# Optimization experiments

Hardware: AMD Instinct MI355X
Metric: run time of the kernel (lower is better)

The kernel has to match this reference:

```python
import jax, jax.numpy as jnp
import numpy as np

N_TOKENS = 8192
EMBED = 1024
HIDDEN = 4 * EMBED
NUM_EXPERTS = 8


def setup_inputs() -> dict:
    key = jax.random.key(0)
    ks = jax.random.split(key, 10)
    s = 0.02
    return {
        "x": jax.random.normal(ks[0], (N_TOKENS, EMBED), dtype=jnp.float32),
        # Router params
        "Wr1": jax.random.normal(ks[1], (EMBED, EMBED), dtype=jnp.float32) * s,
        "br1": jnp.zeros((EMBED,), dtype=jnp.float32),
        "Wr2": jax.random.normal(ks[2], (EMBED, NUM_EXPERTS), dtype=jnp.float32) * s,
        "br2": jnp.zeros((NUM_EXPERTS,), dtype=jnp.float32),
        # Expert FFN params, stacked over experts
        "W1": jax.random.normal(ks[3], (NUM_EXPERTS, EMBED, HIDDEN), dtype=jnp.float32) * s,
        "b1": jnp.zeros((NUM_EXPERTS, HIDDEN), dtype=jnp.float32),
        "W2": jax.random.normal(ks[4], (NUM_EXPERTS, HIDDEN, EMBED), dtype=jnp.float32) * s,
        "b2": jnp.zeros((NUM_EXPERTS, EMBED), dtype=jnp.float32),
    }


def reference(x, Wr1, br1, Wr2, br2, W1, b1, W2, b2):
    # Router: Linear -> ReLU -> Linear -> softmax over experts -> top-1
    h = jax.nn.relu(x @ Wr1 + br1)                      # [N, E]
    probs = jax.nn.softmax(h @ Wr2 + br2, axis=1)       # [N, num_experts]
    chosen = jnp.argmax(probs, axis=1)                  # [N]

    num_experts = W1.shape[0]
    out = jnp.zeros_like(x)
    # Fixed small loop over experts (structurally distinct weights).
    for e in range(num_experts):
        ffn_e = jax.nn.relu(x @ W1[e] + b1[e]) @ W2[e] + b2[e]  # [N, E]
        out = jnp.where((chosen == e)[:, None], ffn_e, out)
    # Note: original returns raw expert output (no probability weighting).
    return out
```

## Files before the change

kernel.cpp:

```cpp
#include <hip/hip_runtime.h>
#include <stdint.h>

#define N_TOK 8192
#define EMB 1024
#define HID 4096
#define NEXP 8

typedef _Float16 f16x8 __attribute__((ext_vector_type(8)));
typedef _Float16 f16x4 __attribute__((ext_vector_type(4)));
typedef short    s16x8 __attribute__((ext_vector_type(8)));
typedef unsigned short u16x8 __attribute__((ext_vector_type(8)));
typedef float    f32x4 __attribute__((ext_vector_type(4)));

typedef __attribute__((address_space(1))) const void gvoid_t;
typedef __attribute__((address_space(3))) void lvoid_t;

__device__ __forceinline__ void async16(const void* g, void* l) {
  __builtin_amdgcn_global_load_lds((gvoid_t*)g, (lvoid_t*)l, 16, 0, 0);
}

__device__ __forceinline__ unsigned short f2bf(float f) {
  unsigned u = __builtin_bit_cast(unsigned, f);
  u += 0x7fffu + ((u >> 16) & 1u);
  return (unsigned short)(u >> 16);
}

__global__ __launch_bounds__(256) void k_cast_x(const float* __restrict__ x,
    unsigned short* __restrict__ xb, _Float16* __restrict__ xhi, _Float16* __restrict__ xlo) {
  int i = (blockIdx.x * 256 + threadIdx.x) << 2;
  float4 v = *(const float4*)(x + i);
  ushort4 b;
  b.x = f2bf(v.x); b.y = f2bf(v.y); b.z = f2bf(v.z); b.w = f2bf(v.w);
  *(ushort4*)(xb + i) = b;
  float vv[4] = {v.x, v.y, v.z, v.w};
  f16x4 hi, lo;
#pragma unroll
  for (int j = 0; j < 4; j++) {
    _Float16 h = (_Float16)vv[j];
    hi[j] = h;
    lo[j] = (_Float16)(vv[j] - (float)h);
  }
  *(f16x4*)(xhi + i) = hi;
  *(f16x4*)(xlo + i) = lo;
}

__global__ __launch_bounds__(256) void k_trans_wr1(const float* __restrict__ src,
    _Float16* __restrict__ dhi, _Float16* __restrict__ dlo) {
  int nblk = blockIdx.x >> 4, kc = blockIdx.x & 15;
  int n = (nblk << 8) + threadIdx.x;
  int k0 = kc << 6;
  for (int k = k0; k < k0 + 64; k += 8) {
    f16x8 hi, lo;
#pragma unroll
    for (int j = 0; j < 8; j++) {
      float w = src[(size_t)(k + j) * EMB + n] * 256.0f;
      _Float16 h = (_Float16)w;
      hi[j] = h;
      lo[j] = (_Float16)(w - (float)h);
    }
    *(f16x8*)(dhi + (size_t)n * EMB + k) = hi;
    *(f16x8*)(dlo + (size_t)n * EMB + k) = lo;
  }
}

__global__ __launch_bounds__(256) void k_transcast_v2(const float* __restrict__ src,
    unsigned short* __restrict__ dst, int K, int Nn, int ktiles, int ntiles) {
  __shared__ __align__(16) unsigned short lds[256 * 72];
  int b = blockIdx.x;
  int e = b / (ktiles * ntiles);
  int r = b % (ktiles * ntiles);
  int kt = r / ntiles, nt = r % ntiles;
  int k0 = kt << 6, n0 = nt << 8;
  const float* s = src + (size_t)e * K * Nn;
  unsigned short* d = dst + (size_t)e * K * Nn;
  int tid = threadIdx.x;
  const float* scol = s + n0 + tid;
#pragma unroll 4
  for (int k = 0; k < 64; k += 2) {
    float a  = scol[(size_t)(k0 + k) * Nn];
    float bv = scol[(size_t)(k0 + k + 1) * Nn];
    unsigned p = (unsigned)f2bf(a) | ((unsigned)f2bf(bv) << 16);
    *(unsigned*)(lds + tid * 72 + k) = p;
  }
  __syncthreads();
  int c = tid & 7, nl = tid >> 3;
#pragma unroll
  for (int p2 = 0; p2 < 8; p2++) {
    int n = (p2 << 5) + nl;
    u16x8 v = *(const u16x8*)(lds + n * 72 + (c << 3));
    *(u16x8*)(d + (size_t)(n0 + n) * K + k0 + (c << 3)) = v;
  }
}

__global__ __launch_bounds__(256) void k_router_gemm(
    const _Float16* __restrict__ Ah, const _Float16* __restrict__ Al,
    const _Float16* __restrict__ Bh, const _Float16* __restrict__ Bl,
    const float* __restrict__ br1, float* __restrict__ hOut) {
  __shared__ __align__(16) _Float16 sAh[4096], sAl[4096], sBh[4096], sBl[4096];
  const int tid = threadIdx.x, lane = tid & 63, wave = tid >> 6;
  const int m0 = (blockIdx.x >> 3) << 7;
  const int n0 = (blockIdx.x & 7) << 7;
  const int srow = (wave << 5) + (lane >> 2);
  const int scol = (lane & 3) << 3;
  const size_t aBase = (size_t)(m0 + srow) * EMB + scol;
  const size_t bBase = (size_t)(n0 + srow) * EMB + scol;
  _Float16* lAh = sAh + (wave << 10);
  _Float16* lAl = sAl + (wave << 10);
  _Float16* lBh = sBh + (wave << 10);
  _Float16* lBl = sBl + (wave << 10);
  const int q = lane >> 4, c = lane & 15;
  const int msub = (wave & 1) << 6, nsub = (wave >> 1) << 6;
  f32x4 acc[4][4];
#pragma unroll
  for (int i = 0; i < 4; i++)
#pragma unroll
    for (int j = 0; j < 4; j++) acc[i][j] = (f32x4){0.f, 0.f, 0.f, 0.f};

  for (int kk = 0; kk < EMB; kk += 32) {
    async16(Ah + aBase + kk, lAh);
    async16(Ah + aBase + 16 * EMB + kk, lAh + 512);
    async16(Al + aBase + kk, lAl);
    async16(Al + aBase + 16 * EMB + kk, lAl + 512);
    async16(Bh + bBase + kk, lBh);
    async16(Bh + bBase + 16 * EMB + kk, lBh + 512);
    async16(Bl + bBase + kk, lBl);
    async16(Bl + bBase + 16 * EMB + kk, lBl + 512);
    __syncthreads();
    f16x8 fah[4], fal[4], fbh[4], fbl[4];
#pragma unroll
    for (int i = 0; i < 4; i++) {
      int ar = msub + (i << 4) + c;
      int br = nsub + (i << 4) + c;
      fah[i] = *(const f16x8*)(sAh + (ar << 5) + (q << 3));
      fal[i] = *(const f16x8*)(sAl + (ar << 5) + (q << 3));
      fbh[i] = *(const f16x8*)(sBh + (br << 5) + (q << 3));
      fbl[i] = *(const f16x8*)(sBl + (br << 5) + (q << 3));
    }
#pragma unroll
    for (int mi = 0; mi < 4; mi++)
#pragma unroll
      for (int ni = 0; ni < 4; ni++) {
        acc[mi][ni] = __builtin_amdgcn_mfma_f32_16x16x32_f16(fah[mi], fbh[ni], acc[mi][ni], 0, 0, 0);
        acc[mi][ni] = __builtin_amdgcn_mfma_f32_16x16x32_f16(fah[mi], fbl[ni], acc[mi][ni], 0, 0, 0);
        acc[mi][ni] = __builtin_amdgcn_mfma_f32_16x16x32_f16(fal[mi], fbh[ni], acc[mi][ni], 0, 0, 0);
      }
    __syncthreads();
  }
#pragma unroll
  for (int mi = 0; mi < 4; mi++)
#pragma unroll
    for (int ni = 0; ni < 4; ni++) {
      int gn = n0 + nsub + (ni << 4) + c;
      float bias = 256.0f * br1[gn];
#pragma unroll
      for (int i2 = 0; i2 < 4; i2++) {
        int gm = m0 + msub + (mi << 4) + (q << 2) + i2;
        float v = acc[mi][ni][i2] + bias;
        hOut[(size_t)gm * EMB + gn] = v > 0.f ? v : 0.f;
      }
    }
}

__global__ __launch_bounds__(256) void k_logits(const float* __restrict__ h,
    const float* __restrict__ Wr2, const float* __restrict__ br2, int* __restrict__ chosen) {
  __shared__ __align__(16) float sW[EMB * NEXP];
  int tid = threadIdx.x;
  for (int i = tid; i < EMB * NEXP; i += 256) sW[i] = Wr2[i];
  __syncthreads();
  int lane = tid & 63, wave = tid >> 6;
  int t = blockIdx.x * 4 + wave;
  const float* hr = h + (size_t)t * EMB;
  float acc[8] = {0.f, 0.f, 0.f, 0.f, 0.f, 0.f, 0.f, 0.f};
#pragma unroll
  for (int i = 0; i < 16; i++) {
    int k = (i << 6) + lane;
    float v = hr[k];
    float4 w0 = *(const float4*)(sW + (k << 3));
    float4 w1 = *(const float4*)(sW + (k << 3) + 4);
    acc[0] += v * w0.x; acc[1] += v * w0.y; acc[2] += v * w0.z; acc[3] += v * w0.w;
    acc[4] += v * w1.x; acc[5] += v * w1.y; acc[6] += v * w1.z; acc[7] += v * w1.w;
  }
#pragma unroll
  for (int off = 32; off > 0; off >>= 1)
#pragma unroll
    for (int e = 0; e < 8; e++) acc[e] += __shfl_down(acc[e], off);
  if (lane == 0) {
    float best = acc[0] + 256.0f * br2[0];
    int bi = 0;
#pragma unroll
    for (int e = 1; e < 8; e++) {
      float l = acc[e] + 256.0f * br2[e];
      if (l > best) { best = l; bi = e; }
    }
    chosen[t] = bi;
  }
}

__global__ void k_zero(int* meta) { meta[threadIdx.x] = 0; }

__global__ __launch_bounds__(256) void k_hist(const int* __restrict__ chosen, int* meta) {
  int i = blockIdx.x * 256 + threadIdx.x;
  atomicAdd(&meta[chosen[i]], 1);
}

__global__ __launch_bounds__(128) void k_sched(int* meta) {
  __shared__ int cnt[8];
  int tid = threadIdx.x;
  if (tid < 8) cnt[tid] = meta[tid];
  __syncthreads();
  int off[9]; off[0] = 0;
#pragma unroll
  for (int e = 0; e < 8; e++) off[e + 1] = off[e] + cnt[e];
  int ts[9]; ts[0] = 0;
#pragma unroll
  for (int e = 0; e < 8; e++) ts[e + 1] = ts[e] + ((cnt[e] + 127) >> 7);
  int T = ts[8];
  if (tid < 8) meta[16 + tid] = off[tid];
  if (tid == 0) { meta[24] = off[8]; meta[25] = T; }
  if (tid < T) {
    int e = 0;
    while (ts[e + 1] <= tid) e++;
    int m = off[e] + ((tid - ts[e]) << 7);
    int end = off[e + 1];
    meta[32 + tid] = e;
    meta[112 + tid] = m;
    meta[192 + tid] = (m + 128 < end) ? m + 128 : end;
  }
}

__global__ __launch_bounds__(256) void k_scatter(const int* __restrict__ chosen,
                                                 int* meta, int* __restrict__ perm) {
  int i = blockIdx.x * 256 + threadIdx.x;
  int e = chosen[i];
  int pos = meta[16 + e] + atomicAdd(&meta[8 + e], 1);
  perm[pos] = i;
}

__global__ __launch_bounds__(256) void k_ffn1(
    const unsigned short* __restrict__ xb, const unsigned short* __restrict__ w1t,
    const float* __restrict__ b1, const int* __restrict__ perm,
    const int* __restrict__ meta, unsigned short* __restrict__ hidden) {
  const int mt = blockIdx.x >> 5;
  if (mt >= meta[25]) return;
  const int nt = blockIdx.x & 31;
  const int e = meta[32 + mt];
  const int row0 = meta[112 + mt];
  const int rend = meta[192 + mt];
  const int n0 = nt << 7;
  __shared__ __align__(16) unsigned short sA[4096], sB[4096];
  const int tid = threadIdx.x, lane = tid & 63, wave = tid >> 6;
  const int srow = (wave << 5) + (lane >> 2);
  const int scol = (lane & 3) << 3;
  int ra0 = row0 + srow, ra1 = row0 + srow + 16;
  if (ra0 > rend - 1) ra0 = rend - 1;
  if (ra1 > rend - 1) ra1 = rend - 1;
  const int t0 = perm[ra0], t1 = perm[ra1];
  const unsigned short* a0 = xb + (size_t)t0 * EMB + scol;
  const unsigned short* a1 = xb + (size_t)t1 * EMB + scol;
  const unsigned short* bsrc = w1t + (size_t)e * EMB * HID + (size_t)(n0 + srow) * EMB + scol;
  unsigned short* lA = sA + (wave << 10);
  unsigned short* lB = sB + (wave << 10);
  const int q = lane >> 4, c = lane & 15;
  const int msub = (wave & 1) << 6, nsub = (wave >> 1) << 6;
  f32x4 acc[4][4];
#pragma unroll
  for (int i = 0; i < 4; i++)
#pragma unroll
    for (int j = 0; j < 4; j++) acc[i][j] = (f32x4){0.f, 0.f, 0.f, 0.f};

  for (int kk = 0; kk < EMB; kk += 32) {
    async16(a0 + kk, lA);
    async16(a1 + kk, lA + 512);
    async16(bsrc + kk, lB);
    async16(bsrc + 16 * EMB + kk, lB + 512);
    __syncthreads();
    s16x8 fa[4], fb[4];
#pragma unroll
    for (int i = 0; i < 4; i++) {
      fa[i] = *(const s16x8*)(sA + ((msub + (i << 4) + c) << 5) + (q << 3));
      fb[i] = *(const s16x8*)(sB + ((nsub + (i << 4) + c) << 5) + (q << 3));
    }
#pragma unroll
    for (int mi = 0; mi < 4; mi++)
#pragma unroll
      for (int ni = 0; ni < 4; ni++)
        acc[mi][ni] = __builtin_amdgcn_mfma_f32_16x16x32_bf16(fa[mi], fb[ni], acc[mi][ni], 0, 0, 0);
    __syncthreads();
  }
#pragma unroll
  for (int mi = 0; mi < 4; mi++)
#pragma unroll
    for (int ni = 0; ni < 4; ni++) {
      int gn = n0 + nsub + (ni << 4) + c;
      float bias = b1[e * HID + gn];
#pragma unroll
      for (int i2 = 0; i2 < 4; i2++) {
        int rs = row0 + msub + (mi << 4) + (q << 2) + i2;
        if (rs < rend) {
          float v = acc[mi][ni][i2] + bias;
          v = v > 0.f ? v : 0.f;
          hidden[(size_t)rs * HID + gn] = f2bf(v);
        }
      }
    }
}

__global__ __launch_bounds__(256) void k_ffn2(
    const unsigned short* __restrict__ hidden, const unsigned short* __restrict__ w2t,
    const float* __restrict__ b2, const int* __restrict__ perm,
    const int* __restrict__ meta, float* __restrict__ out) {
  const int mt = blockIdx.x >> 3;
  if (mt >= meta[25]) return;
  const int nt = blockIdx.x & 7;
  const int e = meta[32 + mt];
  const int row0 = meta[112 + mt];
  const int rend = meta[192 + mt];
  const int n0 = nt << 7;
  __shared__ __align__(16) unsigned short sA[4096], sB[4096];
  const int tid = threadIdx.x, lane = tid & 63, wave = tid >> 6;
  const int srow = (wave << 5) + (lane >> 2);
  const int scol = (lane & 3) << 3;
  int ra0 = row0 + srow, ra1 = row0 + srow + 16;
  if (ra0 > N_TOK - 1) ra0 = N_TOK - 1;
  if (ra1 > N_TOK - 1) ra1 = N_TOK - 1;
  const unsigned short* a0 = hidden + (size_t)ra0 * HID + scol;
  const unsigned short* a1 = hidden + (size_t)ra1 * HID + scol;
  const unsigned short* bsrc = w2t + (size_t)e * HID * EMB + (size_t)(n0 + srow) * HID + scol;
  unsigned short* lA = sA + (wave << 10);
  unsigned short* lB = sB + (wave << 10);
  const int q = lane >> 4, c = lane & 15;
  const int msub = (wave & 1) << 6, nsub = (wave >> 1) << 6;
  f32x4 acc[4][4];
#pragma unroll
  for (int i = 0; i < 4; i++)
#pragma unroll
    for (int j = 0; j < 4; j++) acc[i][j] = (f32x4){0.f, 0.f, 0.f, 0.f};

  for (int kk = 0; kk < HID; kk += 32) {
    async16(a0 + kk, lA);
    async16(a1 + kk, lA + 512);
    async16(bsrc + kk, lB);
    async16(bsrc + 16 * HID + kk, lB + 512);
    __syncthreads();
    s16x8 fa[4], fb[4];
#pragma unroll
    for (int i = 0; i < 4; i++) {
      fa[i] = *(const s16x8*)(sA + ((msub + (i << 4) + c) << 5) + (q << 3));
      fb[i] = *(const s16x8*)(sB + ((nsub + (i << 4) + c) << 5) + (q << 3));
    }
#pragma unroll
    for (int mi = 0; mi < 4; mi++)
#pragma unroll
      for (int ni = 0; ni < 4; ni++)
        acc[mi][ni] = __builtin_amdgcn_mfma_f32_16x16x32_bf16(fa[mi], fb[ni], acc[mi][ni], 0, 0, 0);
    __syncthreads();
  }
#pragma unroll
  for (int mi = 0; mi < 4; mi++)
#pragma unroll
    for (int ni = 0; ni < 4; ni++) {
      int gn = n0 + nsub + (ni << 4) + c;
      float bias = b2[e * EMB + gn];
#pragma unroll
      for (int i2 = 0; i2 < 4; i2++) {
        int rs = row0 + msub + (mi << 4) + (q << 2) + i2;
        if (rs < rend) {
          int orig = perm[rs];
          out[(size_t)orig * EMB + gn] = acc[mi][ni][i2] + bias;
        }
      }
    }
}

extern "C" void kernel_launch(void* const* d_in, const int* in_sizes, int n_in,
                              void* d_out, int out_size, void* d_ws, size_t ws_size,
                              hipStream_t stream) {
  const float* x   = (const float*)d_in[0];
  const float* Wr1 = (const float*)d_in[1];
  const float* br1 = (const float*)d_in[2];
  const float* Wr2 = (const float*)d_in[3];
  const float* br2 = (const float*)d_in[4];
  const float* W1  = (const float*)d_in[5];
  const float* b1  = (const float*)d_in[6];
  const float* W2  = (const float*)d_in[7];
  const float* b2  = (const float*)d_in[8];
  float* out = (float*)d_out;
  char* ws = (char*)d_ws;

  unsigned short* w1t    = (unsigned short*)(ws + 0);
  unsigned short* w2t    = (unsigned short*)(ws + 67108864);
  unsigned short* xb     = (unsigned short*)(ws + 134217728);
  _Float16*       xhi    = (_Float16*)(ws + 150994944);
  _Float16*       xlo    = (_Float16*)(ws + 167772160);
  _Float16*       whi    = (_Float16*)(ws + 184549376);
  _Float16*       wlo    = (_Float16*)(ws + 186646528);
  float*          hbuf   = (float*)(ws + 188743680);
  unsigned short* hidden = (unsigned short*)(ws + 222298112);
  int*            chosen = (int*)(ws + 289406976);
  int*            perm   = (int*)(ws + 289439744);
  int*            meta   = (int*)(ws + 289472512);

  k_cast_x<<<dim3(8192), dim3(256), 0, stream>>>(x, xb, xhi, xlo);
  k_trans_wr1<<<dim3(64), dim3(256), 0, stream>>>(Wr1, whi, wlo);
  k_transcast_v2<<<dim3(2048), dim3(256), 0, stream>>>(W1, w1t, 1024, 4096, 16, 16);
  k_transcast_v2<<<dim3(2048), dim3(256), 0, stream>>>(W2, w2t, 4096, 1024, 64, 4);
  k_router_gemm<<<dim3(512), dim3(256), 0, stream>>>(xhi, xlo, whi, wlo, br1, hbuf);
  k_logits<<<dim3(2048), dim3(256), 0, stream>>>(hbuf, Wr2, br2, chosen);
  k_zero<<<dim3(1), dim3(256), 0, stream>>>(meta);
  k_hist<<<dim3(32), dim3(256), 0, stream>>>(chosen, meta);
  k_sched<<<dim3(1), dim3(128), 0, stream>>>(meta);
  k_scatter<<<dim3(32), dim3(256), 0, stream>>>(chosen, meta, perm);
  k_ffn1<<<dim3(2304), dim3(256), 0, stream>>>(xb, w1t, b1, perm, meta, hidden);
  k_ffn2<<<dim3(576), dim3(256), 0, stream>>>(hidden, w2t, b2, perm, meta, out);
}
```

Baseline: 773.3 us.

## Software-pipeline GEMM loads with multi-buffered LDS and remap block order

Router, FFN1 and FFN2 GEMMs now prefetch the next K-slice into a second (or, for FFN2, a ring of four) LDS buffer via async global-to-LDS loads. Explicit vmcnt waits and raw s_barrier replace __syncthreads so memory latency overlaps MFMA work. Block indices are also remapped so consecutive workgroups spread across N tiles, likely to improve cache sharing across XCDs. The cost is double or quadruple LDS use, which may lower occupancy. FFN2 drops the trailing barrier and relies on the four-buffer ring to avoid overwrite races.

```diff
diff --git a/kernel.cpp b/kernel.cpp
--- a/kernel.cpp
+++ b/kernel.cpp
@@ -96,18 +96,16 @@
     const _Float16* __restrict__ Ah, const _Float16* __restrict__ Al,
     const _Float16* __restrict__ Bh, const _Float16* __restrict__ Bl,
     const float* __restrict__ br1, float* __restrict__ hOut) {
-  __shared__ __align__(16) _Float16 sAh[4096], sAl[4096], sBh[4096], sBl[4096];
+  __shared__ __align__(16) _Float16 sAh[2][4096], sAl[2][4096], sBh[2][4096], sBl[2][4096];
+  const int wg = (blockIdx.x & 7) * 64 + (blockIdx.x >> 3);
   const int tid = threadIdx.x, lane = tid & 63, wave = tid >> 6;
-  const int m0 = (blockIdx.x >> 3) << 7;
-  const int n0 = (blockIdx.x & 7) << 7;
+  const int m0 = (wg >> 3) << 7;
+  const int n0 = (wg & 7) << 7;
   const int srow = (wave << 5) + (lane >> 2);
   const int scol = (lane & 3) << 3;
   const size_t aBase = (size_t)(m0 + srow) * EMB + scol;
   const size_t bBase = (size_t)(n0 + srow) * EMB + scol;
-  _Float16* lAh = sAh + (wave << 10);
-  _Float16* lAl = sAl + (wave << 10);
-  _Float16* lBh = sBh + (wave << 10);
-  _Float16* lBl = sBl + (wave << 10);
+  const int lofs = wave << 10;
   const int q = lane >> 4, c = lane & 15;
   const int msub = (wave & 1) << 6, nsub = (wave >> 1) << 6;
   f32x4 acc[4][4];
@@ -116,25 +114,37 @@
 #pragma unroll
     for (int j = 0; j < 4; j++) acc[i][j] = (f32x4){0.f, 0.f, 0.f, 0.f};
 
-  for (int kk = 0; kk < EMB; kk += 32) {
-    async16(Ah + aBase + kk, lAh);
-    async16(Ah + aBase + 16 * EMB + kk, lAh + 512);
-    async16(Al + aBase + kk, lAl);
-    async16(Al + aBase + 16 * EMB + kk, lAl + 512);
-    async16(Bh + bBase + kk, lBh);
-    async16(Bh + bBase + 16 * EMB + kk, lBh + 512);
-    async16(Bl + bBase + kk, lBl);
-    async16(Bl + bBase + 16 * EMB + kk, lBl + 512);
-    __syncthreads();
+#define RSTAGE(kk, b) do { \
+    async16(Ah + aBase + (kk), sAh[b] + lofs); \
+    async16(Ah + aBase + 16 * EMB + (kk), sAh[b] + lofs + 512); \
+    async16(Al + aBase + (kk), sAl[b] + lofs); \
+    async16(Al + aBase + 16 * EMB + (kk), sAl[b] + lofs + 512); \
+    async16(Bh + bBase + (kk), sBh[b] + lofs); \
+    async16(Bh + bBase + 16 * EMB + (kk), sBh[b] + lofs + 512); \
+    async16(Bl + bBase + (kk), sBl[b] + lofs); \
+    async16(Bl + bBase + 16 * EMB + (kk), sBl[b] + lofs + 512); } while (0)
+
+  RSTAGE(0, 0);
+  const int nk = EMB / 32;
+  for (int t = 0; t < nk; ++t) {
+    const int b = t & 1;
+    if (t + 1 < nk) {
+      RSTAGE((t + 1) << 5, b ^ 1);
+      asm volatile("s_waitcnt vmcnt(8)" ::: "memory");
+    } else {
+      asm volatile("s_waitcnt vmcnt(0)" ::: "memory");
+    }
+    __builtin_amdgcn_s_barrier();
+    asm volatile("" ::: "memory");
     f16x8 fah[4], fal[4], fbh[4], fbl[4];
 #pragma unroll
     for (int i = 0; i < 4; i++) {
       int ar = msub + (i << 4) + c;
       int br = nsub + (i << 4) + c;
-      fah[i] = *(const f16x8*)(sAh + (ar << 5) + (q << 3));
-      fal[i] = *(const f16x8*)(sAl + (ar << 5) + (q << 3));
-      fbh[i] = *(const f16x8*)(sBh + (br << 5) + (q << 3));
-      fbl[i] = *(const f16x8*)(sBl + (br << 5) + (q << 3));
+      fah[i] = *(const f16x8*)(sAh[b] + (ar << 5) + (q << 3));
+      fal[i] = *(const f16x8*)(sAl[b] + (ar << 5) + (q << 3));
+      fbh[i] = *(const f16x8*)(sBh[b] + (br << 5) + (q << 3));
+      fbl[i] = *(const f16x8*)(sBl[b] + (br << 5) + (q << 3));
     }
 #pragma unroll
     for (int mi = 0; mi < 4; mi++)
@@ -144,8 +154,10 @@
         acc[mi][ni] = __builtin_amdgcn_mfma_f32_16x16x32_f16(fah[mi], fbl[ni], acc[mi][ni], 0, 0, 0);
         acc[mi][ni] = __builtin_amdgcn_mfma_f32_16x16x32_f16(fal[mi], fbh[ni], acc[mi][ni], 0, 0, 0);
       }
-    __syncthreads();
-  }
+    asm volatile("" ::: "memory");
+    __builtin_amdgcn_s_barrier();
+  }
+#undef RSTAGE
 #pragma unroll
   for (int mi = 0; mi < 4; mi++)
 #pragma unroll
@@ -240,14 +252,15 @@
     const unsigned short* __restrict__ xb, const unsigned short* __restrict__ w1t,
     const float* __restrict__ b1, const int* __restrict__ perm,
     const int* __restrict__ meta, unsigned short* __restrict__ hidden) {
-  const int mt = blockIdx.x >> 5;
+  const int wg = (blockIdx.x & 7) * 288 + (blockIdx.x >> 3);
+  const int mt = wg >> 5;
   if (mt >= meta[25]) return;
-  const int nt = blockIdx.x & 31;
+  const int nt = wg & 31;
   const int e = meta[32 + mt];
   const int row0 = meta[112 + mt];
   const int rend = meta[192 + mt];
   const int n0 = nt << 7;
-  __shared__ __align__(16) unsigned short sA[4096], sB[4096];
+  __shared__ __align__(16) unsigned short sA[2][4096], sB[2][4096];
   const int tid = threadIdx.x, lane = tid & 63, wave = tid >> 6;
   const int srow = (wave << 5) + (lane >> 2);
   const int scol = (lane & 3) << 3;
@@ -258,8 +271,7 @@
   const unsigned short* a0 = xb + (size_t)t0 * EMB + scol;
   const unsigned short* a1 = xb + (size_t)t1 * EMB + scol;
   const unsigned short* bsrc = w1t + (size_t)e * EMB * HID + (size_t)(n0 + srow) * EMB + scol;
-  unsigned short* lA = sA + (wave << 10);
-  unsigned short* lB = sB + (wave << 10);
+  const int lofs = wave << 10;
   const int q = lane >> 4, c = lane & 15;
   const int msub = (wave & 1) << 6, nsub = (wave >> 1) << 6;
   f32x4 acc[4][4];
@@ -268,25 +280,39 @@
 #pragma unroll
     for (int j = 0; j < 4; j++) acc[i][j] = (f32x4){0.f, 0.f, 0.f, 0.f};
 
-  for (int kk = 0; kk < EMB; kk += 32) {
-    async16(a0 + kk, lA);
-    async16(a1 + kk, lA + 512);
-    async16(bsrc + kk, lB);
-    async16(bsrc + 16 * EMB + kk, lB + 512);
-    __syncthreads();
+#define F1STAGE(kk, b) do { \
+    async16(a0 + (kk), sA[b] + lofs); \
+    async16(a1 + (kk), sA[b] + lofs + 512); \
+    async16(bsrc + (kk), sB[b] + lofs); \
+    async16(bsrc + 16 * EMB + (kk), sB[b] + lofs + 512); } while (0)
+
+  F1STAGE(0, 0);
+  const int nk = EMB / 32;
+  for (int t = 0; t < nk; ++t) {
+    const int b = t & 1;
+    if (t + 1 < nk) {
+      F1STAGE((t + 1) << 5, b ^ 1);
+      asm volatile("s_waitcnt vmcnt(4)" ::: "memory");
+    } else {
+      asm volatile("s_waitcnt vmcnt(0)" ::: "memory");
+    }
+    __builtin_amdgcn_s_barrier();
+    asm volatile("" ::: "memory");
     s16x8 fa[4], fb[4];
 #pragma unroll
     for (int i = 0; i < 4; i++) {
-      fa[i] = *(const s16x8*)(sA + ((msub + (i << 4) + c) << 5) + (q << 3));
-      fb[i] = *(const s16x8*)(sB + ((nsub + (i << 4) + c) << 5) + (q << 3));
+      fa[i] = *(const s16x8*)(sA[b] + ((msub + (i << 4) + c) << 5) + (q << 3));
+      fb[i] = *(const s16x8*)(sB[b] + ((nsub + (i << 4) + c) << 5) + (q << 3));
     }
 #pragma unroll
     for (int mi = 0; mi < 4; mi++)
 #pragma unroll
       for (int ni = 0; ni < 4; ni++)
         acc[mi][ni] = __builtin_amdgcn_mfma_f32_16x16x32_bf16(fa[mi], fb[ni], acc[mi][ni], 0, 0, 0);
-    __syncthreads();
-  }
+    asm volatile("" ::: "memory");
+    __builtin_amdgcn_s_barrier();
+  }
+#undef F1STAGE
 #pragma unroll
   for (int mi = 0; mi < 4; mi++)
 #pragma unroll
@@ -309,14 +335,15 @@
     const unsigned short* __restrict__ hidden, const unsigned short* __restrict__ w2t,
     const float* __restrict__ b2, const int* __restrict__ perm,
     const int* __restrict__ meta, float* __restrict__ out) {
-  const int mt = blockIdx.x >> 3;
+  const int wg = (blockIdx.x & 7) * 72 + (blockIdx.x >> 3);
+  const int mt = wg >> 3;
   if (mt >= meta[25]) return;
-  const int nt = blockIdx.x & 7;
+  const int nt = wg & 7;
   const int e = meta[32 + mt];
   const int row0 = meta[112 + mt];
   const int rend = meta[192 + mt];
   const int n0 = nt << 7;
-  __shared__ __align__(16) unsigned short sA[4096], sB[4096];
+  __shared__ __align__(16) unsigned short sA[4][4096], sB[4][4096];
   const int tid = threadIdx.x, lane = tid & 63, wave = tid >> 6;
   const int srow = (wave << 5) + (lane >> 2);
   const int scol = (lane & 3) << 3;
@@ -326,8 +353,7 @@
   const unsigned short* a0 = hidden + (size_t)ra0 * HID + scol;
   const unsigned short* a1 = hidden + (size_t)ra1 * HID + scol;
   const unsigned short* bsrc = w2t + (size_t)e * HID * EMB + (size_t)(n0 + srow) * HID + scol;
-  unsigned short* lA = sA + (wave << 10);
-  unsigned short* lB = sB + (wave << 10);
+  const int lofs = wave << 10;
   const int q = lane >> 4, c = lane & 15;
   const int msub = (wave & 1) << 6, nsub = (wave >> 1) << 6;
   f32x4 acc[4][4];
@@ -336,25 +362,41 @@
 #pragma unroll
     for (int j = 0; j < 4; j++) acc[i][j] = (f32x4){0.f, 0.f, 0.f, 0.f};
 
-  for (int kk = 0; kk < HID; kk += 32) {
-    async16(a0 + kk, lA);
-    async16(a1 + kk, lA + 512);
-    async16(bsrc + kk, lB);
-    async16(bsrc + 16 * HID + kk, lB + 512);
-    __syncthreads();
+#define F2STAGE(kk, b) do { \
+    async16(a0 + (kk), sA[b] + lofs); \
+    async16(a1 + (kk), sA[b] + lofs + 512); \
+    async16(bsrc + (kk), sB[b] + lofs); \
+    async16(bsrc + 16 * HID + (kk), sB[b] + lofs + 512); } while (0)
+
+  F2STAGE(0, 0);
+  F2STAGE(32, 1);
+  const int nk = HID / 32;
+#pragma unroll 1
+  for (int t = 0; t < nk; ++t) {
+    const int b = t & 3;
+    if (t + 2 < nk) {
+      F2STAGE((t + 2) << 5, (t + 2) & 3);
+      asm volatile("s_waitcnt vmcnt(8)" ::: "memory");
+    } else if (t + 1 < nk) {
+      asm volatile("s_waitcnt vmcnt(4)" ::: "memory");
+    } else {
+      asm volatile("s_waitcnt vmcnt(0)" ::: "memory");
+    }
+    __builtin_amdgcn_s_barrier();
+    asm volatile("" ::: "memory");
     s16x8 fa[4], fb[4];
 #pragma unroll
     for (int i = 0; i < 4; i++) {
-      fa[i] = *(const s16x8*)(sA + ((msub + (i << 4) + c) << 5) + (q << 3));
-      fb[i] = *(const s16x8*)(sB + ((nsub + (i << 4) + c) << 5) + (q << 3));
+      fa[i] = *(const s16x8*)(sA[b] + ((msub + (i << 4) + c) << 5) + (q << 3));
+      fb[i] = *(const s16x8*)(sB[b] + ((nsub + (i << 4) + c) << 5) + (q << 3));
     }
 #pragma unroll
     for (int mi = 0; mi < 4; mi++)
 #pragma unroll
       for (int ni = 0; ni < 4; ni++)
         acc[mi][ni] = __builtin_amdgcn_mfma_f32_16x16x32_bf16(fa[mi], fb[ni], acc[mi][ni], 0, 0, 0);
-    __syncthreads();
-  }
+  }
+#undef F2STAGE
 #pragma unroll
   for (int mi = 0; mi < 4; mi++)
 #pragma unroll
```

After: 823.8 us. 6.5% more time.

## Double-buffer FFN GEMM LDS tiles, XOR-swizzle LDS, remap blocks for L2 locality

Applied to the files above, without the earlier changes.

The FFN1 and FFN2 expert GEMMs now double-buffer their LDS tiles, prefetching the next K-slice with async global-to-LDS loads while MFMAs run on the current one, with one wait and barrier per iteration. Column offsets are XOR-swizzled so fragment reads avoid LDS bank conflicts. FFN2 also doubles its K-step to 64 to halve the number of barriers. Block indices in the router and FFN kernels are remapped so that consecutive blocks spread across eight groups, aiming for better L2 reuse. The cost is twice the LDS per block, which may lower occupancy.

```diff
diff --git a/kernel.cpp b/kernel.cpp
--- a/kernel.cpp
+++ b/kernel.cpp
@@ -97,9 +97,10 @@
     const _Float16* __restrict__ Bh, const _Float16* __restrict__ Bl,
     const float* __restrict__ br1, float* __restrict__ hOut) {
   __shared__ __align__(16) _Float16 sAh[4096], sAl[4096], sBh[4096], sBl[4096];
+  const int wg = (blockIdx.x & 7) * 64 + (blockIdx.x >> 3);
   const int tid = threadIdx.x, lane = tid & 63, wave = tid >> 6;
-  const int m0 = (blockIdx.x >> 3) << 7;
-  const int n0 = (blockIdx.x & 7) << 7;
+  const int m0 = (wg >> 3) << 7;
+  const int n0 = (wg & 7) << 7;
   const int srow = (wave << 5) + (lane >> 2);
   const int scol = (lane & 3) << 3;
   const size_t aBase = (size_t)(m0 + srow) * EMB + scol;
@@ -240,17 +241,18 @@
     const unsigned short* __restrict__ xb, const unsigned short* __restrict__ w1t,
     const float* __restrict__ b1, const int* __restrict__ perm,
     const int* __restrict__ meta, unsigned short* __restrict__ hidden) {
-  const int mt = blockIdx.x >> 5;
+  const int wg = (blockIdx.x & 7) * 288 + (blockIdx.x >> 3);
+  const int mt = wg >> 5;
   if (mt >= meta[25]) return;
-  const int nt = blockIdx.x & 31;
+  const int nt = wg & 31;
   const int e = meta[32 + mt];
   const int row0 = meta[112 + mt];
   const int rend = meta[192 + mt];
   const int n0 = nt << 7;
-  __shared__ __align__(16) unsigned short sA[4096], sB[4096];
+  __shared__ __align__(16) unsigned short sA[2][4096], sB[2][4096];
   const int tid = threadIdx.x, lane = tid & 63, wave = tid >> 6;
   const int srow = (wave << 5) + (lane >> 2);
-  const int scol = (lane & 3) << 3;
+  const int scol = (((lane & 3) ^ ((lane >> 2) & 3)) << 3);
   int ra0 = row0 + srow, ra1 = row0 + srow + 16;
   if (ra0 > rend - 1) ra0 = rend - 1;
   if (ra1 > rend - 1) ra1 = rend - 1;
@@ -258,35 +260,45 @@
   const unsigned short* a0 = xb + (size_t)t0 * EMB + scol;
   const unsigned short* a1 = xb + (size_t)t1 * EMB + scol;
   const unsigned short* bsrc = w1t + (size_t)e * EMB * HID + (size_t)(n0 + srow) * EMB + scol;
-  unsigned short* lA = sA + (wave << 10);
-  unsigned short* lB = sB + (wave << 10);
+  const int lofs = wave << 10;
   const int q = lane >> 4, c = lane & 15;
   const int msub = (wave & 1) << 6, nsub = (wave >> 1) << 6;
+  const int cs = ((q ^ (c & 3)) << 3);
   f32x4 acc[4][4];
 #pragma unroll
   for (int i = 0; i < 4; i++)
 #pragma unroll
     for (int j = 0; j < 4; j++) acc[i][j] = (f32x4){0.f, 0.f, 0.f, 0.f};
 
-  for (int kk = 0; kk < EMB; kk += 32) {
-    async16(a0 + kk, lA);
-    async16(a1 + kk, lA + 512);
-    async16(bsrc + kk, lB);
-    async16(bsrc + 16 * EMB + kk, lB + 512);
-    __syncthreads();
+#define F1STAGE(kk, b) do { \
+    async16(a0 + (kk), sA[b] + lofs); \
+    async16(a1 + (kk), sA[b] + lofs + 512); \
+    async16(bsrc + (kk), sB[b] + lofs); \
+    async16(bsrc + 16 * EMB + (kk), sB[b] + lofs + 512); } while (0)
+
+  F1STAGE(0, 0);
+  asm volatile("s_waitcnt vmcnt(0)" ::: "memory");
+  __builtin_amdgcn_s_barrier();
+  const int nk = EMB / 32;
+#pragma unroll 1
+  for (int t = 0; t < nk; ++t) {
+    const int b = t & 1;
+    if (t + 1 < nk) F1STAGE((t + 1) << 5, b ^ 1);
     s16x8 fa[4], fb[4];
 #pragma unroll
     for (int i = 0; i < 4; i++) {
-      fa[i] = *(const s16x8*)(sA + ((msub + (i << 4) + c) << 5) + (q << 3));
-      fb[i] = *(const s16x8*)(sB + ((nsub + (i << 4) + c) << 5) + (q << 3));
+      fa[i] = *(const s16x8*)(sA[b] + ((msub + (i << 4) + c) << 5) + cs);
+      fb[i] = *(const s16x8*)(sB[b] + ((nsub + (i << 4) + c) << 5) + cs);
     }
 #pragma unroll
     for (int mi = 0; mi < 4; mi++)
 #pragma unroll
       for (int ni = 0; ni < 4; ni++)
         acc[mi][ni] = __builtin_amdgcn_mfma_f32_16x16x32_bf16(fa[mi], fb[ni], acc[mi][ni], 0, 0, 0);
-    __syncthreads();
-  }
+    asm volatile("s_waitcnt vmcnt(0)" ::: "memory");
+    __builtin_amdgcn_s_barrier();
+  }
+#undef F1STAGE
 #pragma unroll
   for (int mi = 0; mi < 4; mi++)
 #pragma unroll
@@ -309,52 +321,78 @@
     const unsigned short* __restrict__ hidden, const unsigned short* __restrict__ w2t,
     const float* __restrict__ b2, const int* __restrict__ perm,
     const int* __restrict__ meta, float* __restrict__ out) {
-  const int mt = blockIdx.x >> 3;
+  const int wg = (blockIdx.x & 7) * 72 + (blockIdx.x >> 3);
+  const int mt = wg >> 3;
   if (mt >= meta[25]) return;
-  const int nt = blockIdx.x & 7;
+  const int nt = wg & 7;
   const int e = meta[32 + mt];
   const int row0 = meta[112 + mt];
   const int rend = meta[192 + mt];
   const int n0 = nt << 7;
-  __shared__ __align__(16) unsigned short sA[4096], sB[4096];
+  __shared__ __align__(16) unsigned short sA[2][8192], sB[2][8192];
   const int tid = threadIdx.x, lane = tid & 63, wave = tid >> 6;
-  const int srow = (wave << 5) + (lane >> 2);
-  const int scol = (lane & 3) << 3;
-  int ra0 = row0 + srow, ra1 = row0 + srow + 16;
-  if (ra0 > N_TOK - 1) ra0 = N_TOK - 1;
-  if (ra1 > N_TOK - 1) ra1 = N_TOK - 1;
-  const unsigned short* a0 = hidden + (size_t)ra0 * HID + scol;
-  const unsigned short* a1 = hidden + (size_t)ra1 * HID + scol;
-  const unsigned short* bsrc = w2t + (size_t)e * HID * EMB + (size_t)(n0 + srow) * HID + scol;
-  unsigned short* lA = sA + (wave << 10);
-  unsigned short* lB = sB + (wave << 10);
+  const int lrow = lane >> 3;
+  const int lcol = (((lane & 7) ^ lrow) << 3);
+  const int lofs = wave << 11;
+  const unsigned short* aptr[4];
+  const unsigned short* bptr[4];
+#pragma unroll
+  for (int j = 0; j < 4; j++) {
+    int ra = row0 + (wave << 5) + (j << 3) + lrow;
+    if (ra > N_TOK - 1) ra = N_TOK - 1;
+    aptr[j] = hidden + (size_t)ra * HID + lcol;
+    bptr[j] = w2t + (size_t)e * HID * EMB
+            + (size_t)(n0 + (wave << 5) + (j << 3) + lrow) * HID + lcol;
+  }
   const int q = lane >> 4, c = lane & 15;
   const int msub = (wave & 1) << 6, nsub = (wave >> 1) << 6;
+  const int cs0 = ((q ^ (c & 7)) << 3);
+  const int cs1 = (((q + 4) ^ (c & 7)) << 3);
   f32x4 acc[4][4];
 #pragma unroll
   for (int i = 0; i < 4; i++)
 #pragma unroll
     for (int j = 0; j < 4; j++) acc[i][j] = (f32x4){0.f, 0.f, 0.f, 0.f};
 
-  for (int kk = 0; kk < HID; kk += 32) {
-    async16(a0 + kk, lA);
-    async16(a1 + kk, lA + 512);
-    async16(bsrc + kk, lB);
-    async16(bsrc + 16 * HID + kk, lB + 512);
-    __syncthreads();
-    s16x8 fa[4], fb[4];
+#define F2STAGE(kk, b) do { \
+    async16(aptr[0] + (kk), sA[b] + lofs); \
+    async16(aptr[1] + (kk), sA[b] + lofs + 512); \
+    async16(aptr[2] + (kk), sA[b] + lofs + 1024); \
+    async16(aptr[3] + (kk), sA[b] + lofs + 1536); \
+    async16(bptr[0] + (kk), sB[b] + lofs); \
+    async16(bptr[1] + (kk), sB[b] + lofs + 512); \
+    async16(bptr[2] + (kk), sB[b] + lofs + 1024); \
+    async16(bptr[3] + (kk), sB[b] + lofs + 1536); } while (0)
+
+  F2STAGE(0, 0);
+  asm volatile("s_waitcnt vmcnt(0)" ::: "memory");
+  __builtin_amdgcn_s_barrier();
+  const int nk = HID / 64;
+#pragma unroll 1
+  for (int t = 0; t < nk; ++t) {
+    const int b = t & 1;
+    if (t + 1 < nk) F2STAGE((t + 1) << 6, b ^ 1);
+    s16x8 fa[2][4], fb[2][4];
 #pragma unroll
     for (int i = 0; i < 4; i++) {
-      fa[i] = *(const s16x8*)(sA + ((msub + (i << 4) + c) << 5) + (q << 3));
-      fb[i] = *(const s16x8*)(sB + ((nsub + (i << 4) + c) << 5) + (q << 3));
+      int arb = (msub + (i << 4) + c) << 6;
+      int brb = (nsub + (i << 4) + c) << 6;
+      fa[0][i] = *(const s16x8*)(sA[b] + arb + cs0);
+      fa[1][i] = *(const s16x8*)(sA[b] + arb + cs1);
+      fb[0][i] = *(const s16x8*)(sB[b] + brb + cs0);
+      fb[1][i] = *(const s16x8*)(sB[b] + brb + cs1);
     }
 #pragma unroll
     for (int mi = 0; mi < 4; mi++)
 #pragma unroll
-      for (int ni = 0; ni < 4; ni++)
-        acc[mi][ni] = __builtin_amdgcn_mfma_f32_16x16x32_bf16(fa[mi], fb[ni], acc[mi][ni], 0, 0, 0);
-    __syncthreads();
-  }
+      for (int ni = 0; ni < 4; ni++) {
+        acc[mi][ni] = __builtin_amdgcn_mfma_f32_16x16x32_bf16(fa[0][mi], fb[0][ni], acc[mi][ni], 0, 0, 0);
+        acc[mi][ni] = __builtin_amdgcn_mfma_f32_16x16x32_bf16(fa[1][mi], fb[1][ni], acc[mi][ni], 0, 0, 0);
+      }
+    asm volatile("s_waitcnt vmcnt(0)" ::: "memory");
+    __builtin_amdgcn_s_barrier();
+  }
+#undef F2STAGE
 #pragma unroll
   for (int mi = 0; mi < 4; mi++)
 #pragma unroll
```

Result: slower. 805.9 us (+4.2%).

## Split-K expert FFN2 with reduce kernel, double-buffer FFN1, swizzle LDS, remap blocks

Applied to the files above, without the earlier changes.

FFN2 now splits its 4096-long reduction into four K-chunks, so it launches four times as many workgroups. The partial sums go to fp32 buffers that reuse dead workspace regions, and a new reduce kernel adds them with the bias and scatters rows back to their original token order. FFN1 gains double-buffered LDS staging with explicit waitcnt/barrier so the next tile's loads overlap the current MFMAs. Both FFN kernels use an XOR column swizzle to reduce LDS bank conflicts. Workgroup IDs are remapped across XCDs for the router GEMM and FFN kernels to improve L2 locality. The cost is the extra partial-sum traffic and one more launch.

```diff
diff --git a/kernel.cpp b/kernel.cpp
--- a/kernel.cpp
+++ b/kernel.cpp
@@ -97,9 +97,10 @@
     const _Float16* __restrict__ Bh, const _Float16* __restrict__ Bl,
     const float* __restrict__ br1, float* __restrict__ hOut) {
   __shared__ __align__(16) _Float16 sAh[4096], sAl[4096], sBh[4096], sBl[4096];
+  const int wg = (blockIdx.x & 7) * 64 + (blockIdx.x >> 3);
   const int tid = threadIdx.x, lane = tid & 63, wave = tid >> 6;
-  const int m0 = (blockIdx.x >> 3) << 7;
-  const int n0 = (blockIdx.x & 7) << 7;
+  const int m0 = (wg >> 3) << 7;
+  const int n0 = (wg & 7) << 7;
   const int srow = (wave << 5) + (lane >> 2);
   const int scol = (lane & 3) << 3;
   const size_t aBase = (size_t)(m0 + srow) * EMB + scol;
@@ -240,17 +241,18 @@
     const unsigned short* __restrict__ xb, const unsigned short* __restrict__ w1t,
     const float* __restrict__ b1, const int* __restrict__ perm,
     const int* __restrict__ meta, unsigned short* __restrict__ hidden) {
-  const int mt = blockIdx.x >> 5;
+  const int wg = (blockIdx.x & 7) * 288 + (blockIdx.x >> 3);
+  const int mt = wg >> 5;
   if (mt >= meta[25]) return;
-  const int nt = blockIdx.x & 31;
+  const int nt = wg & 31;
   const int e = meta[32 + mt];
   const int row0 = meta[112 + mt];
   const int rend = meta[192 + mt];
   const int n0 = nt << 7;
-  __shared__ __align__(16) unsigned short sA[4096], sB[4096];
+  __shared__ __align__(16) unsigned short sA[2][4096], sB[2][4096];
   const int tid = threadIdx.x, lane = tid & 63, wave = tid >> 6;
   const int srow = (wave << 5) + (lane >> 2);
-  const int scol = (lane & 3) << 3;
+  const int scol = (((lane & 3) ^ ((lane >> 2) & 3)) << 3);
   int ra0 = row0 + srow, ra1 = row0 + srow + 16;
   if (ra0 > rend - 1) ra0 = rend - 1;
   if (ra1 > rend - 1) ra1 = rend - 1;
@@ -258,35 +260,45 @@
   const unsigned short* a0 = xb + (size_t)t0 * EMB + scol;
   const unsigned short* a1 = xb + (size_t)t1 * EMB + scol;
   const unsigned short* bsrc = w1t + (size_t)e * EMB * HID + (size_t)(n0 + srow) * EMB + scol;
-  unsigned short* lA = sA + (wave << 10);
-  unsigned short* lB = sB + (wave << 10);
+  const int lofs = wave << 10;
   const int q = lane >> 4, c = lane & 15;
   const int msub = (wave & 1) << 6, nsub = (wave >> 1) << 6;
+  const int cs = ((q ^ (c & 3)) << 3);
   f32x4 acc[4][4];
 #pragma unroll
   for (int i = 0; i < 4; i++)
 #pragma unroll
     for (int j = 0; j < 4; j++) acc[i][j] = (f32x4){0.f, 0.f, 0.f, 0.f};
 
-  for (int kk = 0; kk < EMB; kk += 32) {
-    async16(a0 + kk, lA);
-    async16(a1 + kk, lA + 512);
-    async16(bsrc + kk, lB);
-    async16(bsrc + 16 * EMB + kk, lB + 512);
-    __syncthreads();
+#define F1STAGE(kk, b) do { \
+    async16(a0 + (kk), sA[b] + lofs); \
+    async16(a1 + (kk), sA[b] + lofs + 512); \
+    async16(bsrc + (kk), sB[b] + lofs); \
+    async16(bsrc + 16 * EMB + (kk), sB[b] + lofs + 512); } while (0)
+
+  F1STAGE(0, 0);
+  asm volatile("s_waitcnt vmcnt(0)" ::: "memory");
+  __builtin_amdgcn_s_barrier();
+  const int nk = EMB / 32;
+#pragma unroll 1
+  for (int t = 0; t < nk; ++t) {
+    const int b = t & 1;
+    if (t + 1 < nk) F1STAGE((t + 1) << 5, b ^ 1);
     s16x8 fa[4], fb[4];
 #pragma unroll
     for (int i = 0; i < 4; i++) {
-      fa[i] = *(const s16x8*)(sA + ((msub + (i << 4) + c) << 5) + (q << 3));
-      fb[i] = *(const s16x8*)(sB + ((nsub + (i << 4) + c) << 5) + (q << 3));
+      fa[i] = *(const s16x8*)(sA[b] + ((msub + (i << 4) + c) << 5) + cs);
+      fb[i] = *(const s16x8*)(sB[b] + ((nsub + (i << 4) + c) << 5) + cs);
     }
 #pragma unroll
     for (int mi = 0; mi < 4; mi++)
 #pragma unroll
       for (int ni = 0; ni < 4; ni++)
         acc[mi][ni] = __builtin_amdgcn_mfma_f32_16x16x32_bf16(fa[mi], fb[ni], acc[mi][ni], 0, 0, 0);
-    __syncthreads();
-  }
+    asm volatile("s_waitcnt vmcnt(0)" ::: "memory");
+    __builtin_amdgcn_s_barrier();
+  }
+#undef F1STAGE
 #pragma unroll
   for (int mi = 0; mi < 4; mi++)
 #pragma unroll
@@ -307,36 +319,42 @@
 
 __global__ __launch_bounds__(256) void k_ffn2(
     const unsigned short* __restrict__ hidden, const unsigned short* __restrict__ w2t,
-    const float* __restrict__ b2, const int* __restrict__ perm,
-    const int* __restrict__ meta, float* __restrict__ out) {
-  const int mt = blockIdx.x >> 3;
+    const int* __restrict__ meta,
+    float* __restrict__ p0, float* __restrict__ p1,
+    float* __restrict__ p2, float* __restrict__ p3) {
+  const int wg = (blockIdx.x & 7) * 288 + (blockIdx.x >> 3);
+  const int kc = wg / 576;
+  const int r  = wg % 576;
+  const int mt = r >> 3;
   if (mt >= meta[25]) return;
-  const int nt = blockIdx.x & 7;
+  const int nt = r & 7;
   const int e = meta[32 + mt];
   const int row0 = meta[112 + mt];
   const int rend = meta[192 + mt];
   const int n0 = nt << 7;
+  const int k0 = kc << 10;
   __shared__ __align__(16) unsigned short sA[4096], sB[4096];
   const int tid = threadIdx.x, lane = tid & 63, wave = tid >> 6;
   const int srow = (wave << 5) + (lane >> 2);
-  const int scol = (lane & 3) << 3;
+  const int scol = (((lane & 3) ^ ((lane >> 2) & 3)) << 3);
   int ra0 = row0 + srow, ra1 = row0 + srow + 16;
   if (ra0 > N_TOK - 1) ra0 = N_TOK - 1;
   if (ra1 > N_TOK - 1) ra1 = N_TOK - 1;
-  const unsigned short* a0 = hidden + (size_t)ra0 * HID + scol;
-  const unsigned short* a1 = hidden + (size_t)ra1 * HID + scol;
-  const unsigned short* bsrc = w2t + (size_t)e * HID * EMB + (size_t)(n0 + srow) * HID + scol;
+  const unsigned short* a0 = hidden + (size_t)ra0 * HID + k0 + scol;
+  const unsigned short* a1 = hidden + (size_t)ra1 * HID + k0 + scol;
+  const unsigned short* bsrc = w2t + (size_t)e * HID * EMB + (size_t)(n0 + srow) * HID + k0 + scol;
   unsigned short* lA = sA + (wave << 10);
   unsigned short* lB = sB + (wave << 10);
   const int q = lane >> 4, c = lane & 15;
   const int msub = (wave & 1) << 6, nsub = (wave >> 1) << 6;
+  const int cs = ((q ^ (c & 3)) << 3);
   f32x4 acc[4][4];
 #pragma unroll
   for (int i = 0; i < 4; i++)
 #pragma unroll
     for (int j = 0; j < 4; j++) acc[i][j] = (f32x4){0.f, 0.f, 0.f, 0.f};
 
-  for (int kk = 0; kk < HID; kk += 32) {
+  for (int kk = 0; kk < 1024; kk += 32) {
     async16(a0 + kk, lA);
     async16(a1 + kk, lA + 512);
     async16(bsrc + kk, lB);
@@ -345,8 +363,8 @@
     s16x8 fa[4], fb[4];
 #pragma unroll
     for (int i = 0; i < 4; i++) {
-      fa[i] = *(const s16x8*)(sA + ((msub + (i << 4) + c) << 5) + (q << 3));
-      fb[i] = *(const s16x8*)(sB + ((nsub + (i << 4) + c) << 5) + (q << 3));
+      fa[i] = *(const s16x8*)(sA + ((msub + (i << 4) + c) << 5) + cs);
+      fb[i] = *(const s16x8*)(sB + ((nsub + (i << 4) + c) << 5) + cs);
     }
 #pragma unroll
     for (int mi = 0; mi < 4; mi++)
@@ -355,21 +373,41 @@
         acc[mi][ni] = __builtin_amdgcn_mfma_f32_16x16x32_bf16(fa[mi], fb[ni], acc[mi][ni], 0, 0, 0);
     __syncthreads();
   }
+  float* pout = (kc == 0) ? p0 : (kc == 1) ? p1 : (kc == 2) ? p2 : p3;
 #pragma unroll
   for (int mi = 0; mi < 4; mi++)
 #pragma unroll
     for (int ni = 0; ni < 4; ni++) {
       int gn = n0 + nsub + (ni << 4) + c;
-      float bias = b2[e * EMB + gn];
 #pragma unroll
       for (int i2 = 0; i2 < 4; i2++) {
         int rs = row0 + msub + (mi << 4) + (q << 2) + i2;
-        if (rs < rend) {
-          int orig = perm[rs];
-          out[(size_t)orig * EMB + gn] = acc[mi][ni][i2] + bias;
-        }
+        if (rs < rend) pout[((size_t)rs << 10) + gn] = acc[mi][ni][i2];
       }
     }
+}
+
+__global__ __launch_bounds__(256) void k_reduce(
+    const float* __restrict__ p0, const float* __restrict__ p1,
+    const float* __restrict__ p2, const float* __restrict__ p3,
+    const float* __restrict__ b2, const int* __restrict__ perm,
+    const int* __restrict__ chosen, float* __restrict__ out) {
+  int rs = blockIdx.x;
+  int n = threadIdx.x << 2;
+  int orig = perm[rs];
+  int e = chosen[orig];
+  size_t idx = ((size_t)rs << 10) + n;
+  float4 a = *(const float4*)(p0 + idx);
+  float4 b = *(const float4*)(p1 + idx);
+  float4 c = *(const float4*)(p2 + idx);
+  float4 d = *(const float4*)(p3 + idx);
+  float4 bb = *(const float4*)(b2 + e * EMB + n);
+  float4 rv;
+  rv.x = a.x + b.x + c.x + d.x + bb.x;
+  rv.y = a.y + b.y + c.y + d.y + bb.y;
+  rv.z = a.z + b.z + c.z + d.z + bb.z;
+  rv.w = a.w + b.w + c.w + d.w + bb.w;
+  *(float4*)(out + ((size_t)orig << 10) + n) = rv;
 }
 
 extern "C" void kernel_launch(void* const* d_in, const int* in_sizes, int n_in,
@@ -399,6 +437,10 @@
   int*            chosen = (int*)(ws + 289406976);
   int*            perm   = (int*)(ws + 289439744);
   int*            meta   = (int*)(ws + 289472512);
+  float*          p0     = (float*)(ws + 0);
+  float*          p1     = (float*)(ws + 33554432);
+  float*          p2     = (float*)(ws + 134217728);
+  float*          p3     = (float*)(ws + 167772160);
 
   k_cast_x<<<dim3(8192), dim3(256), 0, stream>>>(x, xb, xhi, xlo);
   k_trans_wr1<<<dim3(64), dim3(256), 0, stream>>>(Wr1, whi, wlo);
@@ -411,5 +453,6 @@
   k_sched<<<dim3(1), dim3(128), 0, stream>>>(meta);
   k_scatter<<<dim3(32), dim3(256), 0, stream>>>(chosen, meta, perm);
   k_ffn1<<<dim3(2304), dim3(256), 0, stream>>>(xb, w1t, b1, perm, meta, hidden);
-  k_ffn2<<<dim3(576), dim3(256), 0, stream>>>(hidden, w2t, b2, perm, meta, out);
-}
+  k_ffn2<<<dim3(2304), dim3(256), 0, stream>>>(hidden, w2t, meta, p0, p1, p2, p3);
+  k_reduce<<<dim3(8192), dim3(256), 0, stream>>>(p0, p1, p2, p3, b2, perm, chosen, out);
+}
```

New measurement: 816.5 us. 5.6% more time.
